# Optimization experiments

Hardware: AMD Instinct MI355X
Metric: run time of the kernel (lower is better)

## Reference

```python
import jax, jax.numpy as jnp
import numpy as np

# Config matching init_kwargs
TAUS = [0.25, 0.5, 0.75]
QWEIGHTS = [0.25, 0.5, 0.25]
T_THRESH = 10
K_DIL = 2
EPS_GIN = 0.0  # (1 + eps) * x term; train_eps=False


def setup_inputs() -> dict:
    key = jax.random.key(0)
    k0, k1, k2, k3 = jax.random.split(key, 4)
    B, N, C, H, CO = 4, 512, 64, 128, 64
    x = jax.random.normal(k0, (B, N, C), dtype=jnp.float32)
    # symmetric random binary adjacency, ~30 avg degree -> dilation active (m > T)
    u = jax.random.uniform(k1, (B, N, N))
    a = (u < 0.03).astype(jnp.float32)
    adj = jnp.maximum(a, jnp.swapaxes(a, 1, 2))
    # last 32 nodes are padding
    mask = jnp.broadcast_to(jnp.arange(N) < (N - 32), (B, N))
    W1 = jax.random.normal(k2, (C, H), dtype=jnp.float32) * (1.0 / np.sqrt(C))
    b1 = jnp.zeros((H,), dtype=jnp.float32)
    W2 = jax.random.normal(k3, (H, CO), dtype=jnp.float32) * (1.0 / np.sqrt(H))
    b2 = jnp.zeros((CO,), dtype=jnp.float32)
    return {"x": x, "adj": adj, "mask": mask, "W1": W1, "b1": b1, "W2": W2, "b2": b2}


def _dilate_adj(adj, mask):
    """Vectorized form of the per-node Python-loop dilation.
    Decisions are based on adj_ (with self-loops), exactly as in the torch loop."""
    B, N, _ = adj.shape
    eye = jnp.eye(N, dtype=bool)
    adj_ = jnp.where(eye[None], 1.0, adj)                 # add self-loops
    nb = (adj_ > 0) & (~eye)[None]                         # neighbors w/o self (B,N,N)
    m = nb.sum(-1)                                         # neighbor count (B,N)
    rank = jnp.cumsum(nb, axis=-1) - 1                     # 0-based position among neighbors
    skip = jnp.where(m > T_THRESH, (m + K_DIL - 1) // K_DIL, 1)  # ceil(m/k); linear mode, layer_idx=1
    do_dil = (skip > 1) & mask                             # masked-out rows are skipped
    removed = nb & do_dil[..., None] & (((rank + 1) % skip[..., None]) == 0)
    rem = removed | jnp.swapaxes(removed, 1, 2)            # symmetric removal
    return jnp.where(rem, 0.0, adj_)


def _weighted_nanquantile_agg(x, valid):
    """Weighted sum of linear-interpolated quantiles over the ragged neighbor dim.
    x: (B,N,C), valid: (B,N,N) bool -> (B,N,C). Empty rows -> 0 (nan_to_num)."""
    B, N, C = x.shape
    big = jnp.finfo(x.dtype).max / 4
    # pool of neighbor features, invalid slots pushed to the end of the sort
    vals = jnp.where(valid[..., None], x[:, None, :, :], big)   # (B,N,N,C)
    sv = jnp.sort(vals, axis=2)
    m = valid.sum(-1)                                           # (B,N)
    mf = m.astype(x.dtype)

    def gather(idx):  # idx (B,N) int -> (B,N,C)
        idxb = jnp.broadcast_to(idx[:, :, None, None], (B, N, 1, C))
        return jnp.take_along_axis(sv, idxb, axis=2)[:, :, 0, :]

    agg = jnp.zeros_like(x)
    for tau, wt in zip(TAUS, QWEIGHTS):
        pos = jnp.clip(tau * (mf - 1.0), 0.0)                   # torch 'linear' interpolation
        lo = jnp.floor(pos).astype(jnp.int32)
        hi = jnp.ceil(pos).astype(jnp.int32)
        frac = (pos - lo.astype(x.dtype))[..., None]
        q = gather(lo) * (1.0 - frac) + gather(hi) * frac
        agg = agg + wt * q
    return jnp.where((m > 0)[..., None], agg, 0.0)


def reference(x, adj, mask, W1, b1, W2, b2):
    dtp = x.dtype
    adj_d = _dilate_adj(adj, mask)
    agg = _weighted_nanquantile_agg(x, adj_d > 0)
    out = (1.0 + EPS_GIN) * x + agg
    h = jax.nn.relu(jnp.einsum('bnc,ch->bnh', out, W1) + b1)    # GIN MLP
    y = jnp.einsum('bnh,ho->bno', h, W2) + b2
    return y * mask[..., None].astype(dtp)
```

## Files before the change

### kernel.cpp

```cpp
#include <hip/hip_runtime.h>
#include <stdint.h>

#define NB 4
#define NN 512
#define NC 64
#define NH 128
#define NCO 64
#define MAXM 64
#define MAXQ 16

__device__ inline bool read_mask(const void* mp, int idx) {
    const int* ip = (const int*)mp;
    int w0 = ip[0];
    if (w0 == 1) return ip[idx] != 0;
    if (w0 == 0x3f800000) return ((const float*)mp)[idx] != 0.0f;
    return ((const unsigned char*)mp)[idx] != 0;
}

__global__ __launch_bounds__(256) void prep_kernel(
        const float* __restrict__ adj, const void* __restrict__ maskp,
        const float* __restrict__ W1, const float* __restrict__ W2,
        uint64_t* __restrict__ validbits, float* __restrict__ W1T,
        float* __restrict__ W2T, int dowt)
{
    int wave = (blockIdx.x * 256 + threadIdx.x) >> 6;
    int lane = threadIdx.x & 63;
    if (wave < NB * NN) {
        int i = wave & (NN - 1);
        const float* arow = adj + (size_t)wave * NN;
        uint64_t ball[8];
        int m = 0;
        #pragma unroll
        for (int k = 0; k < 8; ++k) {
            int j = k * 64 + lane;
            bool f = (j != i) && (arow[j] > 0.0f);
            uint64_t bl = __ballot(f);
            ball[k] = bl;
            m += __popcll(bl);
        }
        int skip = (m > 10) ? ((m + 1) >> 1) : 1;
        bool dodil = (skip > 1) && read_mask(maskp, wave);
        int skip2 = skip * 2;
        int prefix = 0;
        #pragma unroll
        for (int k = 0; k < 8; ++k) {
            uint64_t bl = ball[k];
            int rank1 = prefix + __popcll(bl & ((1ull << lane) - 1ull)) + 1;
            bool f = (bl >> lane) & 1ull;
            bool keep = f && !(dodil && (rank1 == skip || rank1 == skip2));
            uint64_t vb = __ballot(keep);
            if (lane == 0) validbits[(size_t)wave * 8 + k] = vb;
            prefix += __popcll(bl);
        }
    }
    if (dowt) {
        int e = blockIdx.x * 256 + threadIdx.x;
        if (e < 8192) {
            int k = e >> 6, c = e & 63;
            W1T[e] = W1[c * NH + k];
        } else if (e < 16384) {
            int e2 = e - 8192;
            int o = e2 >> 7, k = e2 & 127;
            W2T[e2] = W2[k * NCO + o];
        }
    }
}

template<bool USE_WT>
__global__ __launch_bounds__(256, 8) void fused_kernel(
        const float* __restrict__ x,
        const void* __restrict__ maskp,
        const float* __restrict__ W1,
        const float* __restrict__ b1,
        const float* __restrict__ W2,
        const float* __restrict__ b2,
        const uint64_t* __restrict__ validbits,
        const float* __restrict__ W1T,
        const float* __restrict__ W2T,
        float* __restrict__ out)
{
    int row = blockIdx.x;
    int b = row >> 9, i = row & (NN - 1);
    int tid = threadIdx.x, lane = tid & 63, wv = tid >> 6;
    float* outp = out + (size_t)row * NCO;

    if (!read_mask(maskp, row)) {
        if (tid < NCO) outp[tid] = 0.0f;
        return;
    }

    __shared__ float4 s_q4[NC * MAXQ];
    __shared__ uint16_t s_idx[NN];
    __shared__ float s_qv[NC * 8];
    __shared__ uint64_t s_vb[8];
    __shared__ int s_cnt;

    float xval = (tid < NC) ? x[(size_t)row * NC + tid] : 0.0f;
    if (tid < 8) s_vb[tid] = validbits[(size_t)row * 8 + tid];
    if (tid == 0) { s_cnt = 1; s_idx[0] = (uint16_t)i; }
    __syncthreads();

    int ic = i >> 6;
    uint64_t imask = 1ull << (i & 63);
    #pragma unroll
    for (int it = 0; it < 2; ++it) {
        int j = tid + it * 256;
        if ((s_vb[j >> 6] >> (j & 63)) & 1ull) {
            uint64_t wJ = validbits[((size_t)(b * NN + j)) * 8 + ic];
            if (wJ & imask) {
                int p = atomicAdd(&s_cnt, 1);
                s_idx[p] = (uint16_t)j;
            }
        }
    }
    __syncthreads();
    int m = s_cnt;

    bool fast = (m <= MAXM);
    int mq = (m + 3) >> 2;
    float* sv = (float*)s_q4;
    if (fast) {
        int mq4 = mq << 2;
        for (int j = wv; j < mq4; j += 4) {
            float v = 3.0e38f;
            if (j < m) v = x[((size_t)(b * NN + s_idx[j])) * NC + lane];
            int slot = (j >> 2) ^ (lane & 15);
            sv[lane * 64 + slot * 4 + (j & 3)] = v;
        }
    }
    __syncthreads();

    float mf = (float)m;
    const float taus[3] = {0.25f, 0.5f, 0.75f};
    const float wts[3]  = {0.25f, 0.5f, 0.25f};
    int tlo[3], thi[3];
    float tfrac[3];
    #pragma unroll
    for (int t = 0; t < 3; ++t) {
        float pos = taus[t] * (mf - 1.0f);
        float fl = floorf(pos);
        tlo[t] = (int)fl;
        thi[t] = (int)ceilf(pos);
        tfrac[t] = pos - fl;
    }

    if (fast) {
        const float4* basep = s_q4 + lane * MAXQ;
        int sw = lane & 15;
        for (int ch = wv; ch < mq; ch += 4) {
            float4 q1 = basep[ch ^ sw];
            int rs0 = 0, rs1 = 0, rs2 = 0, rs3 = 0;
            int re0 = 0, re1 = 0, re2 = 0, re3 = 0;
            for (int jq = 0; jq < mq; ++jq) {
                float4 v = basep[jq ^ sw];
                rs0 += (v.x < q1.x) + (v.y < q1.x) + (v.z < q1.x) + (v.w < q1.x);
                re0 += (v.x == q1.x) + (v.y == q1.x) + (v.z == q1.x) + (v.w == q1.x);
                rs1 += (v.x < q1.y) + (v.y < q1.y) + (v.z < q1.y) + (v.w < q1.y);
                re1 += (v.x == q1.y) + (v.y == q1.y) + (v.z == q1.y) + (v.w == q1.y);
                rs2 += (v.x < q1.z) + (v.y < q1.z) + (v.z < q1.z) + (v.w < q1.z);
                re2 += (v.x == q1.z) + (v.y == q1.z) + (v.z == q1.z) + (v.w == q1.z);
                rs3 += (v.x < q1.w) + (v.y < q1.w) + (v.z < q1.w) + (v.w < q1.w);
                re3 += (v.x == q1.w) + (v.y == q1.w) + (v.z == q1.w) + (v.w == q1.w);
            }
            float qe[4] = {q1.x, q1.y, q1.z, q1.w};
            int rsa[4] = {rs0, rs1, rs2, rs3};
            int rea[4] = {re0, re1, re2, re3};
            #pragma unroll
            for (int q = 0; q < 4; ++q) {
                #pragma unroll
                for (int t = 0; t < 3; ++t) {
                    if (rsa[q] <= tlo[t] && tlo[t] < rsa[q] + rea[q])
                        s_qv[lane * 8 + 2 * t] = qe[q];
                    if (rsa[q] <= thi[t] && thi[t] < rsa[q] + rea[q])
                        s_qv[lane * 8 + 2 * t + 1] = qe[q];
                }
            }
        }
    } else if (tid < NC) {
        const float* xb = x + (size_t)b * NN * NC;
        int c = tid;
        for (int j1 = 0; j1 < m; ++j1) {
            float v1 = xb[(size_t)s_idx[j1] * NC + c];
            int rs = 0, re = 0;
            for (int j2 = 0; j2 < m; ++j2) {
                float v2 = xb[(size_t)s_idx[j2] * NC + c];
                rs += v2 < v1;
                re += v2 == v1;
            }
            #pragma unroll
            for (int t = 0; t < 3; ++t) {
                if (rs <= tlo[t] && tlo[t] < rs + re) s_qv[c * 8 + 2 * t] = v1;
                if (rs <= thi[t] && thi[t] < rs + re) s_qv[c * 8 + 2 * t + 1] = v1;
            }
        }
    }
    __syncthreads();

    float* s_mlp  = (float*)s_q4;
    float* s_out  = s_mlp;
    float* s_h    = s_mlp + 64;
    float* s_hp   = s_mlp + 256;
    float* s_part = s_mlp + 512;

    if (tid < NC) {
        float agg = 0.0f;
        #pragma unroll
        for (int t = 0; t < 3; ++t) {
            float q = s_qv[tid * 8 + 2 * t] * (1.0f - tfrac[t])
                    + s_qv[tid * 8 + 2 * t + 1] * tfrac[t];
            agg += wts[t] * q;
        }
        s_out[tid] = xval + agg;
    }
    __syncthreads();

    {
        int k = tid & 127, g = tid >> 7;
        float acc = 0.0f;
        if (USE_WT) {
            const float4* w = (const float4*)(W1T + k * 64 + g * 32);
            #pragma unroll
            for (int q = 0; q < 8; ++q) {
                float4 wq = w[q];
                int cc = g * 32 + q * 4;
                acc += wq.x * s_out[cc] + wq.y * s_out[cc + 1]
                     + wq.z * s_out[cc + 2] + wq.w * s_out[cc + 3];
            }
        } else {
            for (int cc = g * 32; cc < g * 32 + 32; ++cc)
                acc += s_out[cc] * W1[cc * NH + k];
        }
        s_hp[g * NH + k] = acc;
    }
    __syncthreads();
    if (tid < NH) {
        float a = s_hp[tid] + s_hp[NH + tid] + b1[tid];
        s_h[tid] = a > 0.0f ? a : 0.0f;
    }
    __syncthreads();

    {
        int o = tid & 63, g = tid >> 6;
        float acc = 0.0f;
        if (USE_WT) {
            const float4* w = (const float4*)(W2T + o * 128 + g * 32);
            #pragma unroll
            for (int q = 0; q < 8; ++q) {
                float4 wq = w[q];
                int k = g * 32 + q * 4;
                acc += wq.x * s_h[k] + wq.y * s_h[k + 1]
                     + wq.z * s_h[k + 2] + wq.w * s_h[k + 3];
            }
        } else {
            for (int k = g * 32; k < g * 32 + 32; ++k)
                acc += s_h[k] * W2[k * NCO + o];
        }
        s_part[g * NCO + o] = acc;
    }
    __syncthreads();
    if (tid < NCO)
        outp[tid] = s_part[tid] + s_part[64 + tid] + s_part[128 + tid]
                  + s_part[192 + tid] + b2[tid];
}

extern "C" void kernel_launch(void* const* d_in, const int* in_sizes, int n_in,
                              void* d_out, int out_size, void* d_ws, size_t ws_size,
                              hipStream_t stream) {
    const float* x   = (const float*)d_in[0];
    const float* adj = (const float*)d_in[1];
    const void* mask = d_in[2];
    const float* W1  = (const float*)d_in[3];
    const float* b1  = (const float*)d_in[4];
    const float* W2  = (const float*)d_in[5];
    const float* b2  = (const float*)d_in[6];
    float* out = (float*)d_out;

    uint64_t* validbits = (uint64_t*)d_ws;
    float* W1T = (float*)((char*)d_ws + 131072);
    float* W2T = W1T + 8192;
    int dowt = (ws_size >= 196608) ? 1 : 0;

    prep_kernel<<<512, 256, 0, stream>>>(adj, mask, W1, W2, validbits, W1T, W2T, dowt);
    if (dowt)
        fused_kernel<true><<<NB * NN, 256, 0, stream>>>(
            x, mask, W1, b1, W2, b2, validbits, W1T, W2T, out);
    else
        fused_kernel<false><<<NB * NN, 256, 0, stream>>>(
            x, mask, W1, b1, W2, b2, validbits, W1T, W2T, out);
}
```

Measured before the change: 102.3 us.

## Select quantiles via rank-threshold max with atomicMax, wave-aggregated compaction, per-row prep

```diff
diff --git a/kernel.cpp b/kernel.cpp
--- a/kernel.cpp
+++ b/kernel.cpp
@@ -17,42 +17,71 @@
     return ((const unsigned char*)mp)[idx] != 0;
 }
 
+__device__ inline unsigned enc_key(float v) {
+    unsigned b = __float_as_uint(v);
+    return (b & 0x80000000u) ? ~b : (b | 0x80000000u);
+}
+__device__ inline float dec_key(unsigned k) {
+    unsigned b = (k & 0x80000000u) ? (k & 0x7fffffffu) : ~k;
+    return __uint_as_float(b);
+}
+
 __global__ __launch_bounds__(256) void prep_kernel(
         const float* __restrict__ adj, const void* __restrict__ maskp,
         const float* __restrict__ W1, const float* __restrict__ W2,
         uint64_t* __restrict__ validbits, float* __restrict__ W1T,
         float* __restrict__ W2T, int dowt)
 {
-    int wave = (blockIdx.x * 256 + threadIdx.x) >> 6;
-    int lane = threadIdx.x & 63;
-    if (wave < NB * NN) {
-        int i = wave & (NN - 1);
-        const float* arow = adj + (size_t)wave * NN;
-        uint64_t ball[8];
-        int m = 0;
-        #pragma unroll
-        for (int k = 0; k < 8; ++k) {
-            int j = k * 64 + lane;
-            bool f = (j != i) && (arow[j] > 0.0f);
-            uint64_t bl = __ballot(f);
-            ball[k] = bl;
-            m += __popcll(bl);
-        }
-        int skip = (m > 10) ? ((m + 1) >> 1) : 1;
-        bool dodil = (skip > 1) && read_mask(maskp, wave);
-        int skip2 = skip * 2;
-        int prefix = 0;
-        #pragma unroll
-        for (int k = 0; k < 8; ++k) {
-            uint64_t bl = ball[k];
-            int rank1 = prefix + __popcll(bl & ((1ull << lane) - 1ull)) + 1;
-            bool f = (bl >> lane) & 1ull;
-            bool keep = f && !(dodil && (rank1 == skip || rank1 == skip2));
-            uint64_t vb = __ballot(keep);
-            if (lane == 0) validbits[(size_t)wave * 8 + k] = vb;
-            prefix += __popcll(bl);
-        }
-    }
+    __shared__ int s_m[8];
+    int row = blockIdx.x;
+    int tid = threadIdx.x, lane = tid & 63, wv = tid >> 6;
+    int i = row & (NN - 1);
+    const float* arow = adj + (size_t)row * NN;
+
+    uint64_t bl0, bl1;
+    {
+        int j = (wv * 2) * 64 + lane;
+        bool f = (j != i) && (arow[j] > 0.0f);
+        bl0 = __ballot(f);
+    }
+    {
+        int j = (wv * 2 + 1) * 64 + lane;
+        bool f = (j != i) && (arow[j] > 0.0f);
+        bl1 = __ballot(f);
+    }
+    if (lane == 0) {
+        s_m[wv * 2]     = __popcll(bl0);
+        s_m[wv * 2 + 1] = __popcll(bl1);
+    }
+    __syncthreads();
+
+    int m = 0, prefix = 0;
+    #pragma unroll
+    for (int k = 0; k < 8; ++k) {
+        int c = s_m[k];
+        m += c;
+        if (k < wv * 2) prefix += c;
+    }
+    int skip = (m > 10) ? ((m + 1) >> 1) : 1;
+    bool dodil = (skip > 1) && read_mask(maskp, row);
+    int skip2 = skip * 2;
+    uint64_t lanelt = (1ull << lane) - 1ull;
+    {
+        int rank1 = prefix + __popcll(bl0 & lanelt) + 1;
+        bool f = (bl0 >> lane) & 1ull;
+        bool keep = f && !(dodil && (rank1 == skip || rank1 == skip2));
+        uint64_t vb = __ballot(keep);
+        if (lane == 0) validbits[(size_t)row * 8 + wv * 2] = vb;
+        prefix += __popcll(bl0);
+    }
+    {
+        int rank1 = prefix + __popcll(bl1 & lanelt) + 1;
+        bool f = (bl1 >> lane) & 1ull;
+        bool keep = f && !(dodil && (rank1 == skip || rank1 == skip2));
+        uint64_t vb = __ballot(keep);
+        if (lane == 0) validbits[(size_t)row * 8 + wv * 2 + 1] = vb;
+    }
+
     if (dowt) {
         int e = blockIdx.x * 256 + threadIdx.x;
         if (e < 8192) {
@@ -91,7 +120,7 @@
 
     __shared__ float4 s_q4[NC * MAXQ];
     __shared__ uint16_t s_idx[NN];
-    __shared__ float s_qv[NC * 8];
+    __shared__ unsigned s_qk[NC * 6];
     __shared__ uint64_t s_vb[8];
     __shared__ int s_cnt;
 
@@ -102,16 +131,20 @@
 
     int ic = i >> 6;
     uint64_t imask = 1ull << (i & 63);
+    uint64_t lanelt = (1ull << lane) - 1ull;
     #pragma unroll
     for (int it = 0; it < 2; ++it) {
         int j = tid + it * 256;
+        bool hit = false;
         if ((s_vb[j >> 6] >> (j & 63)) & 1ull) {
             uint64_t wJ = validbits[((size_t)(b * NN + j)) * 8 + ic];
-            if (wJ & imask) {
-                int p = atomicAdd(&s_cnt, 1);
-                s_idx[p] = (uint16_t)j;
-            }
-        }
+            hit = (wJ & imask) != 0;
+        }
+        uint64_t bal = __ballot(hit);
+        int base = 0;
+        if (lane == 0 && bal) base = atomicAdd(&s_cnt, __popcll(bal));
+        base = __shfl(base, 0);
+        if (hit) s_idx[base + __popcll(bal & lanelt)] = (uint16_t)j;
     }
     __syncthreads();
     int m = s_cnt;
@@ -128,71 +161,69 @@
             sv[lane * 64 + slot * 4 + (j & 3)] = v;
         }
     }
+    if (tid < NC * 6 / 2) { s_qk[tid] = 0u; s_qk[tid + NC * 3] = 0u; }
     __syncthreads();
 
     float mf = (float)m;
     const float taus[3] = {0.25f, 0.5f, 0.75f};
     const float wts[3]  = {0.25f, 0.5f, 0.25f};
-    int tlo[3], thi[3];
+    int tr[6];
     float tfrac[3];
     #pragma unroll
     for (int t = 0; t < 3; ++t) {
         float pos = taus[t] * (mf - 1.0f);
         float fl = floorf(pos);
-        tlo[t] = (int)fl;
-        thi[t] = (int)ceilf(pos);
+        tr[2 * t]     = (int)fl;
+        tr[2 * t + 1] = (int)ceilf(pos);
         tfrac[t] = pos - fl;
     }
 
     if (fast) {
         const float4* basep = s_q4 + lane * MAXQ;
         int sw = lane & 15;
+        float vmax[6];
+        #pragma unroll
+        for (int t = 0; t < 6; ++t) vmax[t] = -3.0e38f;
         for (int ch = wv; ch < mq; ch += 4) {
             float4 q1 = basep[ch ^ sw];
             int rs0 = 0, rs1 = 0, rs2 = 0, rs3 = 0;
-            int re0 = 0, re1 = 0, re2 = 0, re3 = 0;
             for (int jq = 0; jq < mq; ++jq) {
                 float4 v = basep[jq ^ sw];
                 rs0 += (v.x < q1.x) + (v.y < q1.x) + (v.z < q1.x) + (v.w < q1.x);
-                re0 += (v.x == q1.x) + (v.y == q1.x) + (v.z == q1.x) + (v.w == q1.x);
                 rs1 += (v.x < q1.y) + (v.y < q1.y) + (v.z < q1.y) + (v.w < q1.y);
-                re1 += (v.x == q1.y) + (v.y == q1.y) + (v.z == q1.y) + (v.w == q1.y);
                 rs2 += (v.x < q1.z) + (v.y < q1.z) + (v.z < q1.z) + (v.w < q1.z);
-                re2 += (v.x == q1.z) + (v.y == q1.z) + (v.z == q1.z) + (v.w == q1.z);
                 rs3 += (v.x < q1.w) + (v.y < q1.w) + (v.z < q1.w) + (v.w < q1.w);
-                re3 += (v.x == q1.w) + (v.y == q1.w) + (v.z == q1.w) + (v.w == q1.w);
             }
             float qe[4] = {q1.x, q1.y, q1.z, q1.w};
             int rsa[4] = {rs0, rs1, rs2, rs3};
-            int rea[4] = {re0, re1, re2, re3};
             #pragma unroll
             for (int q = 0; q < 4; ++q) {
                 #pragma unroll
-                for (int t = 0; t < 3; ++t) {
-                    if (rsa[q] <= tlo[t] && tlo[t] < rsa[q] + rea[q])
-                        s_qv[lane * 8 + 2 * t] = qe[q];
-                    if (rsa[q] <= thi[t] && thi[t] < rsa[q] + rea[q])
-                        s_qv[lane * 8 + 2 * t + 1] = qe[q];
-                }
+                for (int t = 0; t < 6; ++t)
+                    vmax[t] = fmaxf(vmax[t], (rsa[q] <= tr[t]) ? qe[q] : -3.0e38f);
             }
         }
+        unsigned* qk = s_qk + lane * 6;
+        #pragma unroll
+        for (int t = 0; t < 6; ++t) atomicMax(qk + t, enc_key(vmax[t]));
     } else if (tid < NC) {
         const float* xb = x + (size_t)b * NN * NC;
         int c = tid;
+        float vmax[6];
+        #pragma unroll
+        for (int t = 0; t < 6; ++t) vmax[t] = -3.0e38f;
         for (int j1 = 0; j1 < m; ++j1) {
             float v1 = xb[(size_t)s_idx[j1] * NC + c];
-            int rs = 0, re = 0;
-            for (int j2 = 0; j2 < m; ++j2) {
-                float v2 = xb[(size_t)s_idx[j2] * NC + c];
-                rs += v2 < v1;
-                re += v2 == v1;
-            }
+            int rs = 0;
+            for (int j2 = 0; j2 < m; ++j2)
+                rs += xb[(size_t)s_idx[j2] * NC + c] < v1;
             #pragma unroll
-            for (int t = 0; t < 3; ++t) {
-                if (rs <= tlo[t] && tlo[t] < rs + re) s_qv[c * 8 + 2 * t] = v1;
-                if (rs <= thi[t] && thi[t] < rs + re) s_qv[c * 8 + 2 * t + 1] = v1;
-            }
-        }
+            for (int t = 0; t < 6; ++t)
+                vmax[t] = fmaxf(vmax[t], (rs <= tr[t]) ? v1 : -3.0e38f);
+        }
+        unsigned* qk = s_qk + c * 6;
+        #pragma unroll
+        for (int t = 0; t < 6; ++t) atomicMax(qk + t, enc_key(vmax[t]));
     }
     __syncthreads();
 
@@ -206,9 +237,9 @@
         float agg = 0.0f;
         #pragma unroll
         for (int t = 0; t < 3; ++t) {
-            float q = s_qv[tid * 8 + 2 * t] * (1.0f - tfrac[t])
-                    + s_qv[tid * 8 + 2 * t + 1] * tfrac[t];
-            agg += wts[t] * q;
+            float qlo = dec_key(s_qk[tid * 6 + 2 * t]);
+            float qhi = dec_key(s_qk[tid * 6 + 2 * t + 1]);
+            agg += wts[t] * (qlo * (1.0f - tfrac[t]) + qhi * tfrac[t]);
         }
         s_out[tid] = xval + agg;
     }
@@ -280,7 +311,7 @@
     float* W2T = W1T + 8192;
     int dowt = (ws_size >= 196608) ? 1 : 0;
 
-    prep_kernel<<<512, 256, 0, stream>>>(adj, mask, W1, W2, validbits, W1T, W2T, dowt);
+    prep_kernel<<<NB * NN, 256, 0, stream>>>(adj, mask, W1, W2, validbits, W1T, W2T, dowt);
     if (dowt)
         fused_kernel<true><<<NB * NN, 256, 0, stream>>>(
             x, mask, W1, b1, W2, b2, validbits, W1T, W2T, out);
```

Result: faster. 96.43 us (-5.7%).
